# Kernel optimization log

Hardware: AMD Instinct MI355X
Metric: run time of the kernel (lower is better)

The kernel has to match this reference:

```python
import jax, jax.numpy as jnp
import numpy as np

EPS = 1e-12  # torch F.normalize eps


def setup_inputs() -> dict:
    key = jax.random.key(0)
    ks = jax.random.split(key, 6)
    B, D, C, N = 4096, 512, 17, 100000
    return {
        "feature": jax.random.normal(ks[0], (B, D), dtype=jnp.float32),
        "clf_w": jax.random.normal(ks[1], (C, D), dtype=jnp.float32),
        "clf_b": jax.random.normal(ks[2], (C,), dtype=jnp.float32),
        "supports": jax.random.normal(ks[3], (N, D), dtype=jnp.float32),
        "ent_bank": jax.random.uniform(ks[4], (N,), dtype=jnp.float32),
        "labels_idx": jax.random.randint(ks[5], (N,), 0, C, dtype=jnp.int64),
        "filter_K": 2048,
    }


def reference(feature, clf_w, clf_b, supports, ent_bank, labels_idx, filter_K):
    C = clf_w.shape[0]
    # classifier logits on the incoming batch
    p = feature @ clf_w.T + clf_b                       # [B, C]
    logp = jax.nn.log_softmax(p, axis=1)
    ent_new = -jnp.sum(jnp.exp(logp) * logp, axis=1)    # softmax entropy [B]
    yhat_idx = jnp.argmax(p, axis=1)                    # pseudo-labels [B]

    # grow the support bank
    sup = jnp.concatenate([supports, feature], axis=0)              # [N+B, D]
    y_hat = jnp.concatenate([labels_idx.astype(jnp.int32),
                             yhat_idx.astype(jnp.int32)], axis=0)   # [N+B]
    ent = jnp.concatenate([ent_bank, ent_new], axis=0)              # [N+B]

    # normalize supports once (select-then-normalize == normalize-then-select)
    sup_n = sup / jnp.maximum(jnp.linalg.norm(sup, axis=1, keepdims=True), EPS)

    # per-class lowest-entropy top-K select; one-hot labels make
    # supports.T @ labels a per-class sum of selected normalized supports.
    def per_class(c):
        ent_c = jnp.where(y_hat == c, ent, jnp.inf)
        neg_top, idx = jax.lax.top_k(-ent_c, filter_K)   # K smallest entropies
        valid = jnp.isfinite(neg_top).astype(sup_n.dtype)  # class may have < K
        return jnp.sum(sup_n[idx] * valid[:, None], axis=0)  # [D]

    Wc = jax.vmap(per_class)(jnp.arange(C))             # [C, D]
    weights = Wc.T                                      # [D, C]
    w_norm = weights / jnp.maximum(jnp.linalg.norm(weights, axis=0, keepdims=True), EPS)
    return feature @ w_norm                             # [B, C]
```

## Files before the change

### kernel.cpp

```cpp
#include <hip/hip_runtime.h>
#include <math.h>
#include <limits.h>

#define D 512
#define C 17
#define CAP 2048
#define CANDCAP 2048
#define PAD 64

__global__ __launch_bounds__(256) void k_front(
    const float* __restrict__ feature, const float* __restrict__ clf_w,
    const float* __restrict__ clf_b, const float* __restrict__ ent_bank,
    const int* __restrict__ labels, float* __restrict__ ent_new,
    int* __restrict__ yhat, unsigned* __restrict__ hist16,
    unsigned* __restrict__ ghist8, int N, int B)
{
    __shared__ float w_s[C * D];
    __shared__ float b_s[C];
    int tid = threadIdx.x;
    for (int i = tid; i < C * D; i += 256) w_s[i] = clf_w[i];
    if (tid < C) b_s[tid] = clf_b[tid];
    __syncthreads();
    int wave = tid >> 6, lane = tid & 63;

    int row = blockIdx.x * 4 + wave;
    if (row < B) {
        const float* f = feature + (size_t)row * D;
        float4 f0 = *(const float4*)(f + lane * 8);
        float4 f1 = *(const float4*)(f + lane * 8 + 4);
        double p[C];
        for (int c = 0; c < C; ++c) {
            const float* w = w_s + c * D + lane * 8;
            double s = (double)f0.x * w[0] + (double)f0.y * w[1] +
                       (double)f0.z * w[2] + (double)f0.w * w[3] +
                       (double)f1.x * w[4] + (double)f1.y * w[5] +
                       (double)f1.z * w[6] + (double)f1.w * w[7];
            for (int m = 32; m; m >>= 1) s += __shfl_xor(s, m, 64);
            p[c] = s + (double)b_s[c];
        }
        if (lane == 0) {
            double mx = p[0]; int am = 0;
            for (int c = 1; c < C; ++c) if (p[c] > mx) { mx = p[c]; am = c; }
            double Z = 0.0, S = 0.0;
            for (int c = 0; c < C; ++c) {
                double e = exp(p[c] - mx);
                Z += e; S += e * (p[c] - mx);
            }
            float ent = (float)(log(Z) - S / Z);
            ent_new[row] = ent;
            yhat[row] = am;
            unsigned b = __float_as_uint(ent);
            atomicAdd(&hist16[(size_t)am * 65536 + (b >> 16)], 1u);
            atomicAdd(&ghist8[am * 256 + (b >> 24)], 1u);
        }
    }

    int gtid = blockIdx.x * 256 + tid;
    int nchunk = N >> 2;
    if (gtid < nchunk) {
        int4 y4 = *(const int4*)(labels + gtid * 4);
        float4 e4 = *(const float4*)(ent_bank + gtid * 4);
        unsigned b;
        b = __float_as_uint(e4.x);
        atomicAdd(&hist16[(size_t)y4.x * 65536 + (b >> 16)], 1u);
        atomicAdd(&ghist8[y4.x * 256 + (b >> 24)], 1u);
        b = __float_as_uint(e4.y);
        atomicAdd(&hist16[(size_t)y4.y * 65536 + (b >> 16)], 1u);
        atomicAdd(&ghist8[y4.y * 256 + (b >> 24)], 1u);
        b = __float_as_uint(e4.z);
        atomicAdd(&hist16[(size_t)y4.z * 65536 + (b >> 16)], 1u);
        atomicAdd(&ghist8[y4.z * 256 + (b >> 24)], 1u);
        b = __float_as_uint(e4.w);
        atomicAdd(&hist16[(size_t)y4.w * 65536 + (b >> 16)], 1u);
        atomicAdd(&ghist8[y4.w * 256 + (b >> 24)], 1u);
    }
    if (blockIdx.x == 0) {
        for (int i = (nchunk << 2) + tid; i < N; i += 256) {
            int y = labels[i];
            unsigned b = __float_as_uint(ent_bank[i]);
            atomicAdd(&hist16[(size_t)y * 65536 + (b >> 16)], 1u);
            atomicAdd(&ghist8[y * 256 + (b >> 24)], 1u);
        }
    }
}

__device__ inline void wave_rank256(const unsigned h[4], int K, int lane,
                                    int* out_bin, int* out_excl, unsigned* out_total)
{
    unsigned lsum = h[0] + h[1] + h[2] + h[3];
    unsigned x = lsum;
    for (int off = 1; off < 64; off <<= 1) {
        unsigned t = __shfl_up(x, off, 64);
        if (lane >= off) x += t;
    }
    *out_total = __shfl((int)x, 63, 64);
    unsigned excl = x - lsum;
    int myb = -1; int mye = 0;
    unsigned run = excl;
    for (int k = 0; k < 4; ++k) {
        unsigned inc = run + h[k];
        if ((int)run < K && K <= (int)inc) { myb = lane * 4 + k; mye = (int)run; }
        run = inc;
    }
    unsigned long long m = __ballot(myb >= 0);
    int src = (int)__ffsll((unsigned long long)m) - 1;
    *out_bin  = __shfl(myb, src, 64);
    *out_excl = __shfl(mye, src, 64);
}

__global__ __launch_bounds__(256) void k_compact(
    const float* __restrict__ ent_bank, const int* __restrict__ labels,
    const float* __restrict__ ent_new, const int* __restrict__ yhat,
    const unsigned* __restrict__ ghist8, const unsigned* __restrict__ hist16,
    const int* __restrict__ fk, int* __restrict__ krem_g,
    int* __restrict__ cnt_g, int* __restrict__ list,
    unsigned* __restrict__ ccnt_g, unsigned* __restrict__ candb,
    int* __restrict__ candi, int N, int B)
{
    __shared__ unsigned pfx16[C];
    __shared__ int krem_s[C];
    __shared__ int done_s[C];
    __shared__ int lcnt[C], lofs[C], lput[C], gbase[C];
    __shared__ int l_list[1024 + 8];

    int tid = threadIdx.x, wave = tid >> 6, lane = tid & 63;
    int K = fk[0];

    for (int c = wave; c < C; c += 4) {
        uint4 g0 = *(const uint4*)(ghist8 + c * 256 + lane * 4);
        unsigned h[4] = { g0.x, g0.y, g0.z, g0.w };
        int chunk, e1; unsigned total;
        wave_rank256(h, K, lane, &chunk, &e1, &total);
        if ((int)total <= K) {
            if (lane == 0) { done_s[c] = 1; krem_s[c] = 0; pfx16[c] = 0xFFFFFFFFu; }
            continue;
        }
        int K2 = K - e1;
        uint4 g1 = *(const uint4*)(hist16 + (size_t)c * 65536 + chunk * 256 + lane * 4);
        unsigned h2[4] = { g1.x, g1.y, g1.z, g1.w };
        int bin, e2; unsigned tot2;
        wave_rank256(h2, K2, lane, &bin, &e2, &tot2);
        if (lane == 0) {
            done_s[c] = 0;
            pfx16[c] = (unsigned)(chunk * 256 + bin);
            krem_s[c] = K2 - e2;
        }
    }
    if (tid < C) { lcnt[tid] = 0; }
    __syncthreads();
    if (blockIdx.x == 0 && tid < C) krem_g[tid] = krem_s[tid];

    int NT = N + B;
    int nchunk = NT >> 2;
    int gtid = blockIdx.x * 256 + tid;
    int4 y4; uint4 b4; int i0 = gtid << 2; int vn = 0;
    if (gtid < nchunk) {
        vn = 4;
        if (i0 + 4 <= N) {
            y4 = *(const int4*)(labels + i0);
            float4 e = *(const float4*)(ent_bank + i0);
            b4 = make_uint4(__float_as_uint(e.x), __float_as_uint(e.y),
                            __float_as_uint(e.z), __float_as_uint(e.w));
        } else if (i0 >= N) {
            y4 = *(const int4*)(yhat + (i0 - N));
            float4 e = *(const float4*)(ent_new + (i0 - N));
            b4 = make_uint4(__float_as_uint(e.x), __float_as_uint(e.y),
                            __float_as_uint(e.z), __float_as_uint(e.w));
        } else {
            int ys[4]; unsigned bs[4];
            for (int k = 0; k < 4; ++k) {
                int i = i0 + k;
                ys[k] = (i < N) ? labels[i] : yhat[i - N];
                bs[k] = __float_as_uint((i < N) ? ent_bank[i] : ent_new[i - N]);
            }
            y4 = make_int4(ys[0], ys[1], ys[2], ys[3]);
            b4 = make_uint4(bs[0], bs[1], bs[2], bs[3]);
        }
    }
    int y_t = 0; unsigned b_t = 0; int i_t = 0; int have_t = 0;
    int tail0 = nchunk << 2;
    if (blockIdx.x == 0 && tail0 + tid < NT) {
        i_t = tail0 + tid;
        y_t = (i_t < N) ? labels[i_t] : yhat[i_t - N];
        b_t = __float_as_uint((i_t < N) ? ent_bank[i_t] : ent_new[i_t - N]);
        have_t = 1;
    }

    auto each = [&](auto&& g) {
        if (vn > 0) { g(y4.x, b4.x, i0 + 0); g(y4.y, b4.y, i0 + 1);
                      g(y4.z, b4.z, i0 + 2); g(y4.w, b4.w, i0 + 3); }
        if (have_t) g(y_t, b_t, i_t);
    };

    each([&](int y, unsigned b, int i) {
        (void)i;
        unsigned t16 = b >> 16;
        if (done_s[y] || t16 < pfx16[y]) atomicAdd(&lcnt[y], 1);
    });
    __syncthreads();
    if (tid == 0) {
        int run = 0;
        for (int c = 0; c < C; ++c) { lofs[c] = run; run += lcnt[c]; }
    }
    __syncthreads();
    if (tid < C) {
        gbase[tid] = atomicAdd(&cnt_g[tid * PAD], lcnt[tid]);
        lput[tid] = lofs[tid];
    }
    __syncthreads();
    each([&](int y, unsigned b, int i) {
        unsigned t16 = b >> 16;
        if (done_s[y] || t16 < pfx16[y]) {
            int p = atomicAdd(&lput[y], 1);
            l_list[p] = i;
        } else if (t16 == pfx16[y]) {
            unsigned q = atomicAdd(&ccnt_g[y * PAD], 1u);
            if (q < CANDCAP) { candb[y * CANDCAP + q] = b; candi[y * CANDCAP + q] = i; }
        }
    });
    __syncthreads();
    for (int c = 0; c < C; ++c) {
        int m = lcnt[c], base = gbase[c], off = lofs[c];
        for (int t = tid; t < m; t += 256)
            list[c * CAP + base + t] = l_list[off + t];
    }
}

__global__ __launch_bounds__(256) void k_accum(
    const float* __restrict__ supports, const float* __restrict__ feature,
    const int* __restrict__ list, const int* __restrict__ cnt_g,
    const unsigned* __restrict__ ccnt_g, const unsigned* __restrict__ candb,
    const int* __restrict__ candi, const int* __restrict__ krem_g,
    float* __restrict__ Wc, int N)
{
    __shared__ float wsum[4][D];
    __shared__ unsigned cb_s[CANDCAP];
    __shared__ int ci_s[CANDCAP];
    __shared__ int win[CANDCAP];
    __shared__ int wn_s;

    int c = blockIdx.y;
    int s = min(cnt_g[c * PAD], CAP);
    int nch = gridDim.x;
    int R = (s + nch - 1) / nch;
    int start = blockIdx.x * R;
    int end = min(start + R, s);
    int lane = threadIdx.x & 63, wave = threadIdx.x >> 6;
    float a0 = 0.f, a1 = 0.f, a2 = 0.f, a3 = 0.f;
    float a4 = 0.f, a5 = 0.f, a6 = 0.f, a7 = 0.f;

    auto add_row = [&](int r) {
        const float* x = (r < N) ? (supports + (size_t)r * D)
                                 : (feature + (size_t)(r - N) * D);
        float4 p = *(const float4*)(x + lane * 8);
        float4 q = *(const float4*)(x + lane * 8 + 4);
        float ss = p.x * p.x + p.y * p.y + p.z * p.z + p.w * p.w +
                   q.x * q.x + q.y * q.y + q.z * q.z + q.w * q.w;
        for (int m = 32; m; m >>= 1) ss += __shfl_xor(ss, m, 64);
        float inv = 1.f / fmaxf(sqrtf(ss), 1e-12f);
        a0 += p.x * inv; a1 += p.y * inv; a2 += p.z * inv; a3 += p.w * inv;
        a4 += q.x * inv; a5 += q.y * inv; a6 += q.z * inv; a7 += q.w * inv;
    };

    for (int j = start + wave; j < end; j += 4) add_row(list[c * CAP + j]);

    if (blockIdx.x == 0) {
        int n = (int)min(ccnt_g[c * PAD], (unsigned)CANDCAP);
        int Kr = krem_g[c];
        if (n > 0 && Kr > 0) {
            if (threadIdx.x == 0) wn_s = 0;
            for (int j = threadIdx.x; j < n; j += 256) {
                cb_s[j] = candb[c * CANDCAP + j];
                ci_s[j] = candi[c * CANDCAP + j];
            }
            __syncthreads();
            for (int j = threadIdx.x; j < n; j += 256) {
                unsigned bj = cb_s[j]; int ij = ci_s[j];
                int r = 0;
                for (int k = 0; k < n; ++k) {
                    unsigned bk = cb_s[k]; int ik = ci_s[k];
                    r += (bk < bj || (bk == bj && ik < ij)) ? 1 : 0;
                }
                if (r < Kr) { int pos = atomicAdd(&wn_s, 1); win[pos] = ij; }
            }
            __syncthreads();
            int wn = wn_s;
            for (int j = wave; j < wn; j += 4) add_row(win[j]);
        }
    }

    *(float4*)&wsum[wave][lane * 8]     = make_float4(a0, a1, a2, a3);
    *(float4*)&wsum[wave][lane * 8 + 4] = make_float4(a4, a5, a6, a7);
    __syncthreads();
    for (int i = threadIdx.x; i < D; i += 256) {
        float t = wsum[0][i] + wsum[1][i] + wsum[2][i] + wsum[3][i];
        if (t != 0.f) atomicAdd(&Wc[c * D + i], t);
    }
}

__global__ __launch_bounds__(256) void k_out(
    const float* __restrict__ feature, const float* __restrict__ Wc,
    float* __restrict__ out, int B)
{
    __shared__ float w_s[C * D];
    __shared__ float inv_s[C];
    int tid = threadIdx.x;
    for (int i = tid; i < C * D; i += 256) w_s[i] = Wc[i];
    __syncthreads();
    int wave = tid >> 6, lane = tid & 63;
    for (int c = wave; c < C; c += 4) {
        const float* w = w_s + c * D + lane * 8;
        float ss = 0.f;
        for (int k = 0; k < 8; ++k) ss += w[k] * w[k];
        for (int m = 32; m; m >>= 1) ss += __shfl_xor(ss, m, 64);
        if (lane == 0) inv_s[c] = 1.f / fmaxf(sqrtf(ss), 1e-12f);
    }
    __syncthreads();
    for (int row = blockIdx.x * 4 + wave; row < B; row += gridDim.x * 4) {
        const float* f = feature + (size_t)row * D;
        float4 f0 = *(const float4*)(f + lane * 8);
        float4 f1 = *(const float4*)(f + lane * 8 + 4);
        for (int c = 0; c < C; ++c) {
            const float* w = w_s + c * D + lane * 8;
            float s = f0.x * w[0] + f0.y * w[1] + f0.z * w[2] + f0.w * w[3] +
                      f1.x * w[4] + f1.y * w[5] + f1.z * w[6] + f1.w * w[7];
            for (int m = 32; m; m >>= 1) s += __shfl_xor(s, m, 64);
            if (lane == 0) out[(size_t)row * C + c] = s * inv_s[c];
        }
    }
}

extern "C" void kernel_launch(void* const* d_in, const int* in_sizes, int n_in,
                              void* d_out, int out_size, void* d_ws, size_t ws_size,
                              hipStream_t stream)
{
    (void)n_in; (void)out_size; (void)ws_size;
    const float* feature  = (const float*)d_in[0];
    const float* clf_w    = (const float*)d_in[1];
    const float* clf_b    = (const float*)d_in[2];
    const float* supports = (const float*)d_in[3];
    const float* ent_bank = (const float*)d_in[4];
    const int*   labels   = (const int*)d_in[5];
    const int*   fk       = (const int*)d_in[6];
    int B  = in_sizes[0] / D;
    int N  = in_sizes[4];
    int NT = N + B;

    char* ws = (char*)d_ws;
    size_t o = 0;
    auto align256 = [&](size_t x) { return (x + 255) & ~(size_t)255; };
    unsigned* hist16  = (unsigned*)(ws + o); o = align256(o + (size_t)C * 65536 * 4);
    unsigned* ghist8  = (unsigned*)(ws + o); o = align256(o + (size_t)C * 256 * 4);
    float*    Wc      = (float*)(ws + o);    o = align256(o + (size_t)C * D * 4);
    int*      cnt_g   = (int*)(ws + o);      o = align256(o + (size_t)C * PAD * 4);
    unsigned* ccnt_g  = (unsigned*)(ws + o); o = align256(o + (size_t)C * PAD * 4);
    size_t zero_bytes = o;
    float*    ent_new = (float*)(ws + o);    o = align256(o + (size_t)B * 4);
    int*      yhat    = (int*)(ws + o);      o = align256(o + (size_t)B * 4);
    int*      krem_g  = (int*)(ws + o);      o = align256(o + 32 * 4);
    int*      list    = (int*)(ws + o);      o = align256(o + (size_t)C * CAP * 4);
    unsigned* candb   = (unsigned*)(ws + o); o = align256(o + (size_t)C * CANDCAP * 4);
    int*      candi   = (int*)(ws + o);      o = align256(o + (size_t)C * CANDCAP * 4);
    float*    out     = (float*)d_out;

    hipMemsetAsync(ws, 0, zero_bytes, stream);

    int cb = (B + 3) / 4; if (cb > 1024) cb = 1024;
    int fb = cb; int bankb = ((N >> 2) + 255) / 256; if (bankb > fb) fb = bankb;
    int sgc = ((NT >> 2) + 255) / 256;

    k_front<<<fb, 256, 0, stream>>>(feature, clf_w, clf_b, ent_bank, labels,
                                    ent_new, yhat, hist16, ghist8, N, B);
    k_compact<<<sgc, 256, 0, stream>>>(ent_bank, labels, ent_new, yhat,
                                       ghist8, hist16, fk, krem_g,
                                       cnt_g, list, ccnt_g, candb, candi, N, B);
    k_accum<<<dim3(32, C), 256, 0, stream>>>(supports, feature, list, cnt_g,
                                             ccnt_g, candb, candi, krem_g, Wc, N);
    k_out<<<cb, 256, 0, stream>>>(feature, Wc, out, B);
}
```

Before: 359.4 us.

## Fuse pipeline into single cooperative kernel with grid-wide syncs

Replaces the four separate launches (front, compact, accum, out) with one cooperative kernel of 256 persistent blocks separated by grid.sync barriers. It also keeps the coarse 8-bit histogram in shared memory per block and flushes it with one atomic per nonzero bin. Boundary-candidate selection moves into its own phase, where one block per class ranks candidates in parallel into a second list. The final output stage normalizes the class weights once in shared memory, in two halves. The aim is to cut launch gaps and global atomic contention, at the cost of limiting parallelism to a fixed grid and adding grid-wide barrier overhead. The old multi-kernel path remains as a fallback if the cooperative launch fails.

```diff
diff --git a/kernel.cpp b/kernel.cpp
--- a/kernel.cpp
+++ b/kernel.cpp
@@ -1,12 +1,342 @@
 #include <hip/hip_runtime.h>
+#include <hip/hip_cooperative_groups.h>
 #include <math.h>
-#include <limits.h>
+
+namespace cg = cooperative_groups;
 
 #define D 512
 #define C 17
 #define CAP 2048
 #define CANDCAP 2048
 #define PAD 64
+#define GRID 256
+
+__device__ inline void wave_rank256(const unsigned h[4], int K, int lane,
+                                    int* out_bin, int* out_excl, unsigned* out_total)
+{
+    unsigned lsum = h[0] + h[1] + h[2] + h[3];
+    unsigned x = lsum;
+    for (int off = 1; off < 64; off <<= 1) {
+        unsigned t = __shfl_up(x, off, 64);
+        if (lane >= off) x += t;
+    }
+    *out_total = __shfl((int)x, 63, 64);
+    unsigned excl = x - lsum;
+    int myb = -1; int mye = 0;
+    unsigned run = excl;
+    for (int k = 0; k < 4; ++k) {
+        unsigned inc = run + h[k];
+        if ((int)run < K && K <= (int)inc) { myb = lane * 4 + k; mye = (int)run; }
+        run = inc;
+    }
+    unsigned long long m = __ballot(myb >= 0);
+    int src = (int)__ffsll((unsigned long long)m) - 1;
+    *out_bin  = __shfl(myb, src, 64);
+    *out_excl = __shfl(mye, src, 64);
+}
+
+struct KParams {
+    const float* feature; const float* clf_w; const float* clf_b;
+    const float* supports; const float* ent_bank; const int* labels;
+    const int* fk;
+    float* ent_new; int* yhat;
+    unsigned* hist16; unsigned* ghist8; float* Wc;
+    int* cnt_g; unsigned* ccnt_g; int* krem_g; int* s2cnt;
+    int* list; int* list2; unsigned* candb; int* candi;
+    float* out; int N; int B;
+};
+
+union SMem {
+    struct { unsigned h8[C * 256]; } p1;
+    struct { unsigned pfx16[C]; int krem_s[C]; int done_s[C];
+             int lcnt[C]; int lofs[C]; int lput[C]; int gbase[C];
+             int l_list[1312]; } p2;
+    struct { unsigned cb[CANDCAP]; int ci[CANDCAP]; } p3;
+    struct { float wsum[4][D]; } p4;
+    struct { float w_s[9 * D]; float inv_s[32]; } p5;
+};
+
+__global__ __launch_bounds__(256, 1) void k_fused(KParams P)
+{
+    cg::grid_group grid = cg::this_grid();
+    __shared__ SMem sm;
+
+    const int tid = threadIdx.x, bid = blockIdx.x;
+    const int gtid = bid * 256 + tid;
+    const int gsz = GRID * 256;
+    const int wave = tid >> 6, lane = tid & 63;
+    const int gwave = bid * 4 + wave, nwave = GRID * 4;
+    const int N = P.N, B = P.B, NT = N + B;
+
+    {
+        for (int i = tid; i < C * 256; i += 256) sm.p1.h8[i] = 0;
+        __syncthreads();
+
+        for (int row = gwave; row < B; row += nwave) {
+            const float* f = P.feature + (size_t)row * D;
+            float4 f0 = *(const float4*)(f + lane * 8);
+            float4 f1 = *(const float4*)(f + lane * 8 + 4);
+            double p[C];
+            for (int c = 0; c < C; ++c) {
+                const float* w = P.clf_w + c * D + lane * 8;
+                double s = (double)f0.x * w[0] + (double)f0.y * w[1] +
+                           (double)f0.z * w[2] + (double)f0.w * w[3] +
+                           (double)f1.x * w[4] + (double)f1.y * w[5] +
+                           (double)f1.z * w[6] + (double)f1.w * w[7];
+                for (int m = 32; m; m >>= 1) s += __shfl_xor(s, m, 64);
+                p[c] = s + (double)P.clf_b[c];
+            }
+            if (lane == 0) {
+                double mx = p[0]; int am = 0;
+                for (int c = 1; c < C; ++c) if (p[c] > mx) { mx = p[c]; am = c; }
+                double Z = 0.0, S = 0.0;
+                for (int c = 0; c < C; ++c) {
+                    double e = exp(p[c] - mx);
+                    Z += e; S += e * (p[c] - mx);
+                }
+                float ent = (float)(log(Z) - S / Z);
+                P.ent_new[row] = ent;
+                P.yhat[row] = am;
+                unsigned b = __float_as_uint(ent);
+                atomicAdd(&P.hist16[(size_t)am * 65536 + (b >> 16)], 1u);
+                atomicAdd(&P.ghist8[am * 256 + (b >> 24)], 1u);
+            }
+        }
+
+        int nbch = N >> 2;
+        for (int j = gtid; j < nbch; j += gsz) {
+            int4 y4 = *(const int4*)(P.labels + j * 4);
+            float4 e4 = *(const float4*)(P.ent_bank + j * 4);
+            unsigned b;
+            b = __float_as_uint(e4.x);
+            atomicAdd(&P.hist16[(size_t)y4.x * 65536 + (b >> 16)], 1u);
+            atomicAdd(&sm.p1.h8[y4.x * 256 + (b >> 24)], 1u);
+            b = __float_as_uint(e4.y);
+            atomicAdd(&P.hist16[(size_t)y4.y * 65536 + (b >> 16)], 1u);
+            atomicAdd(&sm.p1.h8[y4.y * 256 + (b >> 24)], 1u);
+            b = __float_as_uint(e4.z);
+            atomicAdd(&P.hist16[(size_t)y4.z * 65536 + (b >> 16)], 1u);
+            atomicAdd(&sm.p1.h8[y4.z * 256 + (b >> 24)], 1u);
+            b = __float_as_uint(e4.w);
+            atomicAdd(&P.hist16[(size_t)y4.w * 65536 + (b >> 16)], 1u);
+            atomicAdd(&sm.p1.h8[y4.w * 256 + (b >> 24)], 1u);
+        }
+        if (bid == 0) {
+            for (int i = (nbch << 2) + tid; i < N; i += 256) {
+                int y = P.labels[i];
+                unsigned b = __float_as_uint(P.ent_bank[i]);
+                atomicAdd(&P.hist16[(size_t)y * 65536 + (b >> 16)], 1u);
+                atomicAdd(&P.ghist8[y * 256 + (b >> 24)], 1u);
+            }
+        }
+        __syncthreads();
+        for (int i = tid; i < C * 256; i += 256) {
+            unsigned v = sm.p1.h8[i];
+            if (v) atomicAdd(&P.ghist8[i], v);
+        }
+    }
+    __threadfence(); grid.sync(); __threadfence();
+
+    {
+        int K = P.fk[0];
+        for (int c = wave; c < C; c += 4) {
+            uint4 g0 = *(const uint4*)(P.ghist8 + c * 256 + lane * 4);
+            unsigned h[4] = { g0.x, g0.y, g0.z, g0.w };
+            int chunk, e1; unsigned total;
+            wave_rank256(h, K, lane, &chunk, &e1, &total);
+            if ((int)total <= K) {
+                if (lane == 0) { sm.p2.done_s[c] = 1; sm.p2.krem_s[c] = 0;
+                                 sm.p2.pfx16[c] = 0xFFFFFFFFu; }
+                continue;
+            }
+            int K2 = K - e1;
+            uint4 g1 = *(const uint4*)(P.hist16 + (size_t)c * 65536 + chunk * 256 + lane * 4);
+            unsigned h2[4] = { g1.x, g1.y, g1.z, g1.w };
+            int bin, e2; unsigned tot2;
+            wave_rank256(h2, K2, lane, &bin, &e2, &tot2);
+            if (lane == 0) {
+                sm.p2.done_s[c] = 0;
+                sm.p2.pfx16[c] = (unsigned)(chunk * 256 + bin);
+                sm.p2.krem_s[c] = K2 - e2;
+            }
+        }
+        if (tid < C) sm.p2.lcnt[tid] = 0;
+        __syncthreads();
+        if (bid == 0 && tid < C) P.krem_g[tid] = sm.p2.krem_s[tid];
+
+        int nchunk = NT >> 2;
+        int4 y4; uint4 b4; int i0 = gtid << 2; int vn = 0;
+        if (gtid < nchunk) {
+            vn = 4;
+            if (i0 + 4 <= N) {
+                y4 = *(const int4*)(P.labels + i0);
+                float4 e = *(const float4*)(P.ent_bank + i0);
+                b4 = make_uint4(__float_as_uint(e.x), __float_as_uint(e.y),
+                                __float_as_uint(e.z), __float_as_uint(e.w));
+            } else if (i0 >= N) {
+                y4 = *(const int4*)(P.yhat + (i0 - N));
+                float4 e = *(const float4*)(P.ent_new + (i0 - N));
+                b4 = make_uint4(__float_as_uint(e.x), __float_as_uint(e.y),
+                                __float_as_uint(e.z), __float_as_uint(e.w));
+            } else {
+                int ys[4]; unsigned bs[4];
+                for (int k = 0; k < 4; ++k) {
+                    int i = i0 + k;
+                    ys[k] = (i < N) ? P.labels[i] : P.yhat[i - N];
+                    bs[k] = __float_as_uint((i < N) ? P.ent_bank[i] : P.ent_new[i - N]);
+                }
+                y4 = make_int4(ys[0], ys[1], ys[2], ys[3]);
+                b4 = make_uint4(bs[0], bs[1], bs[2], bs[3]);
+            }
+        }
+        int y_t = 0; unsigned b_t = 0; int i_t = 0; int have_t = 0;
+        int tail0 = nchunk << 2;
+        if (bid == 0 && tail0 + tid < NT) {
+            i_t = tail0 + tid;
+            y_t = (i_t < N) ? P.labels[i_t] : P.yhat[i_t - N];
+            b_t = __float_as_uint((i_t < N) ? P.ent_bank[i_t] : P.ent_new[i_t - N]);
+            have_t = 1;
+        }
+        auto each = [&](auto&& g) {
+            if (vn > 0) { g(y4.x, b4.x, i0 + 0); g(y4.y, b4.y, i0 + 1);
+                          g(y4.z, b4.z, i0 + 2); g(y4.w, b4.w, i0 + 3); }
+            if (have_t) g(y_t, b_t, i_t);
+        };
+
+        each([&](int y, unsigned b, int i) {
+            (void)i;
+            unsigned t16 = b >> 16;
+            if (sm.p2.done_s[y] || t16 < sm.p2.pfx16[y]) atomicAdd(&sm.p2.lcnt[y], 1);
+        });
+        __syncthreads();
+        if (tid == 0) {
+            int run = 0;
+            for (int c = 0; c < C; ++c) { sm.p2.lofs[c] = run; run += sm.p2.lcnt[c]; }
+        }
+        __syncthreads();
+        if (tid < C) {
+            int m = sm.p2.lcnt[tid];
+            sm.p2.gbase[tid] = m ? atomicAdd(&P.cnt_g[tid * PAD], m) : 0;
+            sm.p2.lput[tid] = sm.p2.lofs[tid];
+        }
+        __syncthreads();
+        each([&](int y, unsigned b, int i) {
+            unsigned t16 = b >> 16;
+            if (sm.p2.done_s[y] || t16 < sm.p2.pfx16[y]) {
+                int p = atomicAdd(&sm.p2.lput[y], 1);
+                sm.p2.l_list[p] = i;
+            } else if (t16 == sm.p2.pfx16[y]) {
+                unsigned q = atomicAdd(&P.ccnt_g[y * PAD], 1u);
+                if (q < CANDCAP) { P.candb[y * CANDCAP + q] = b;
+                                   P.candi[y * CANDCAP + q] = i; }
+            }
+        });
+        __syncthreads();
+        for (int c = 0; c < C; ++c) {
+            int m = sm.p2.lcnt[c], base = sm.p2.gbase[c], off = sm.p2.lofs[c];
+            int lim = CAP - base; if (m > lim) m = lim;
+            for (int t = tid; t < m; t += 256)
+                P.list[c * CAP + base + t] = sm.p2.l_list[off + t];
+        }
+    }
+    __threadfence(); grid.sync(); __threadfence();
+
+    if (bid < C) {
+        int c = bid;
+        int Kr = P.krem_g[c];
+        int n = (int)min(P.ccnt_g[c * PAD], (unsigned)CANDCAP);
+        if (Kr > 0 && n > 0) {
+            for (int j = tid; j < n; j += 256) {
+                sm.p3.cb[j] = __hip_atomic_load(&P.candb[c * CANDCAP + j],
+                                  __ATOMIC_RELAXED, __HIP_MEMORY_SCOPE_AGENT);
+                sm.p3.ci[j] = __hip_atomic_load(&P.candi[c * CANDCAP + j],
+                                  __ATOMIC_RELAXED, __HIP_MEMORY_SCOPE_AGENT);
+            }
+            __syncthreads();
+            for (int j = tid; j < n; j += 256) {
+                unsigned bj = sm.p3.cb[j]; int ij = sm.p3.ci[j];
+                int r = 0;
+                for (int k = 0; k < n; ++k) {
+                    unsigned bk = sm.p3.cb[k]; int ik = sm.p3.ci[k];
+                    r += (bk < bj || (bk == bj && ik < ij)) ? 1 : 0;
+                }
+                if (r < Kr) P.list2[c * CANDCAP + r] = ij;
+            }
+        }
+        if (tid == 0) P.s2cnt[c] = (Kr > 0) ? min(Kr, n) : 0;
+    }
+    __threadfence(); grid.sync(); __threadfence();
+
+    {
+        int c = bid % C;
+        int q = bid / C;
+        int nch = (GRID - c + C - 1) / C;
+        int s = min(P.cnt_g[c * PAD], CAP);
+        int R = (s + nch - 1) / nch;
+        int start = q * R;
+        int end = min(start + R, s);
+        float a0 = 0.f, a1 = 0.f, a2 = 0.f, a3 = 0.f;
+        float a4 = 0.f, a5 = 0.f, a6 = 0.f, a7 = 0.f;
+        auto add_row = [&](int r) {
+            const float* x = (r < N) ? (P.supports + (size_t)r * D)
+                                     : (P.feature + (size_t)(r - N) * D);
+            float4 pp = *(const float4*)(x + lane * 8);
+            float4 qq = *(const float4*)(x + lane * 8 + 4);
+            float ss = pp.x * pp.x + pp.y * pp.y + pp.z * pp.z + pp.w * pp.w +
+                       qq.x * qq.x + qq.y * qq.y + qq.z * qq.z + qq.w * qq.w;
+            for (int m = 32; m; m >>= 1) ss += __shfl_xor(ss, m, 64);
+            float inv = 1.f / fmaxf(sqrtf(ss), 1e-12f);
+            a0 += pp.x * inv; a1 += pp.y * inv; a2 += pp.z * inv; a3 += pp.w * inv;
+            a4 += qq.x * inv; a5 += qq.y * inv; a6 += qq.z * inv; a7 += qq.w * inv;
+        };
+        const int* lp = P.list + c * CAP;
+        for (int j = start + wave; j < end; j += 4) add_row(lp[j]);
+        if (q == 0) {
+            int s2 = P.s2cnt[c];
+            for (int j = wave; j < s2; j += 4) add_row(P.list2[c * CANDCAP + j]);
+        }
+        *(float4*)&sm.p4.wsum[wave][lane * 8]     = make_float4(a0, a1, a2, a3);
+        *(float4*)&sm.p4.wsum[wave][lane * 8 + 4] = make_float4(a4, a5, a6, a7);
+        __syncthreads();
+        for (int i = tid; i < D; i += 256) {
+            float t = sm.p4.wsum[0][i] + sm.p4.wsum[1][i] +
+                      sm.p4.wsum[2][i] + sm.p4.wsum[3][i];
+            if (t != 0.f) atomicAdd(&P.Wc[c * D + i], t);
+        }
+    }
+    __threadfence(); grid.sync(); __threadfence();
+
+    {
+        for (int c = wave; c < C; c += 4) {
+            const float* w = P.Wc + c * D + lane * 8;
+            float ss = 0.f;
+            for (int k = 0; k < 8; ++k) ss += w[k] * w[k];
+            for (int m = 32; m; m >>= 1) ss += __shfl_xor(ss, m, 64);
+            if (lane == 0) sm.p5.inv_s[c] = 1.f / fmaxf(sqrtf(ss), 1e-12f);
+        }
+        __syncthreads();
+        for (int half = 0; half < 2; ++half) {
+            int c0 = half * 9, c1 = (half == 0) ? 9 : C;
+            int nc = c1 - c0;
+            for (int i = tid; i < nc * D; i += 256)
+                sm.p5.w_s[i] = P.Wc[c0 * D + i] * sm.p5.inv_s[c0 + i / D];
+            __syncthreads();
+            for (int row = gwave; row < B; row += nwave) {
+                const float* f = P.feature + (size_t)row * D;
+                float4 f0 = *(const float4*)(f + lane * 8);
+                float4 f1 = *(const float4*)(f + lane * 8 + 4);
+                for (int c = 0; c < nc; ++c) {
+                    const float* w = sm.p5.w_s + c * D + lane * 8;
+                    float s = f0.x * w[0] + f0.y * w[1] + f0.z * w[2] + f0.w * w[3] +
+                              f1.x * w[4] + f1.y * w[5] + f1.z * w[6] + f1.w * w[7];
+                    for (int m = 32; m; m >>= 1) s += __shfl_xor(s, m, 64);
+                    if (lane == 0) P.out[(size_t)row * C + c0 + c] = s;
+                }
+            }
+            __syncthreads();
+        }
+    }
+}
 
 __global__ __launch_bounds__(256) void k_front(
     const float* __restrict__ feature, const float* __restrict__ clf_w,
@@ -16,13 +346,12 @@
     unsigned* __restrict__ ghist8, int N, int B)
 {
     __shared__ float w_s[C * D];
-    __shared__ float b_s[C];
+    __shared__ float b_s[32];
     int tid = threadIdx.x;
     for (int i = tid; i < C * D; i += 256) w_s[i] = clf_w[i];
     if (tid < C) b_s[tid] = clf_b[tid];
     __syncthreads();
     int wave = tid >> 6, lane = tid & 63;
-
     int row = blockIdx.x * 4 + wave;
     if (row < B) {
         const float* f = feature + (size_t)row * D;
@@ -54,7 +383,6 @@
             atomicAdd(&ghist8[am * 256 + (b >> 24)], 1u);
         }
     }
-
     int gtid = blockIdx.x * 256 + tid;
     int nchunk = N >> 2;
     if (gtid < nchunk) {
@@ -84,30 +412,6 @@
     }
 }
 
-__device__ inline void wave_rank256(const unsigned h[4], int K, int lane,
-                                    int* out_bin, int* out_excl, unsigned* out_total)
-{
-    unsigned lsum = h[0] + h[1] + h[2] + h[3];
-    unsigned x = lsum;
-    for (int off = 1; off < 64; off <<= 1) {
-        unsigned t = __shfl_up(x, off, 64);
-        if (lane >= off) x += t;
-    }
-    *out_total = __shfl((int)x, 63, 64);
-    unsigned excl = x - lsum;
-    int myb = -1; int mye = 0;
-    unsigned run = excl;
-    for (int k = 0; k < 4; ++k) {
-        unsigned inc = run + h[k];
-        if ((int)run < K && K <= (int)inc) { myb = lane * 4 + k; mye = (int)run; }
-        run = inc;
-    }
-    unsigned long long m = __ballot(myb >= 0);
-    int src = (int)__ffsll((unsigned long long)m) - 1;
-    *out_bin  = __shfl(myb, src, 64);
-    *out_excl = __shfl(mye, src, 64);
-}
-
 __global__ __launch_bounds__(256) void k_compact(
     const float* __restrict__ ent_bank, const int* __restrict__ labels,
     const float* __restrict__ ent_new, const int* __restrict__ yhat,
@@ -121,11 +425,10 @@
     __shared__ int krem_s[C];
     __shared__ int done_s[C];
     __shared__ int lcnt[C], lofs[C], lput[C], gbase[C];
-    __shared__ int l_list[1024 + 8];
+    __shared__ int l_list[1312];
 
     int tid = threadIdx.x, wave = tid >> 6, lane = tid & 63;
     int K = fk[0];
-
     for (int c = wave; c < C; c += 4) {
         uint4 g0 = *(const uint4*)(ghist8 + c * 256 + lane * 4);
         unsigned h[4] = { g0.x, g0.y, g0.z, g0.w };
@@ -146,7 +449,7 @@
             krem_s[c] = K2 - e2;
         }
     }
-    if (tid < C) { lcnt[tid] = 0; }
+    if (tid < C) lcnt[tid] = 0;
     __syncthreads();
     if (blockIdx.x == 0 && tid < C) krem_g[tid] = krem_s[tid];
 
@@ -185,13 +488,11 @@
         b_t = __float_as_uint((i_t < N) ? ent_bank[i_t] : ent_new[i_t - N]);
         have_t = 1;
     }
-
     auto each = [&](auto&& g) {
         if (vn > 0) { g(y4.x, b4.x, i0 + 0); g(y4.y, b4.y, i0 + 1);
                       g(y4.z, b4.z, i0 + 2); g(y4.w, b4.w, i0 + 3); }
         if (have_t) g(y_t, b_t, i_t);
     };
-
     each([&](int y, unsigned b, int i) {
         (void)i;
         unsigned t16 = b >> 16;
@@ -204,7 +505,8 @@
     }
     __syncthreads();
     if (tid < C) {
-        gbase[tid] = atomicAdd(&cnt_g[tid * PAD], lcnt[tid]);
+        int m = lcnt[tid];
+        gbase[tid] = m ? atomicAdd(&cnt_g[tid * PAD], m) : 0;
         lput[tid] = lofs[tid];
     }
     __syncthreads();
@@ -221,6 +523,7 @@
     __syncthreads();
     for (int c = 0; c < C; ++c) {
         int m = lcnt[c], base = gbase[c], off = lofs[c];
+        int lim = CAP - base; if (m > lim) m = lim;
         for (int t = tid; t < m; t += 256)
             list[c * CAP + base + t] = l_list[off + t];
     }
@@ -248,7 +551,6 @@
     int lane = threadIdx.x & 63, wave = threadIdx.x >> 6;
     float a0 = 0.f, a1 = 0.f, a2 = 0.f, a3 = 0.f;
     float a4 = 0.f, a5 = 0.f, a6 = 0.f, a7 = 0.f;
-
     auto add_row = [&](int r) {
         const float* x = (r < N) ? (supports + (size_t)r * D)
                                  : (feature + (size_t)(r - N) * D);
@@ -261,9 +563,7 @@
         a0 += p.x * inv; a1 += p.y * inv; a2 += p.z * inv; a3 += p.w * inv;
         a4 += q.x * inv; a5 += q.y * inv; a6 += q.z * inv; a7 += q.w * inv;
     };
-
     for (int j = start + wave; j < end; j += 4) add_row(list[c * CAP + j]);
-
     if (blockIdx.x == 0) {
         int n = (int)min(ccnt_g[c * PAD], (unsigned)CANDCAP);
         int Kr = krem_g[c];
@@ -288,7 +588,6 @@
             for (int j = wave; j < wn; j += 4) add_row(win[j]);
         }
     }
-
     *(float4*)&wsum[wave][lane * 8]     = make_float4(a0, a1, a2, a3);
     *(float4*)&wsum[wave][lane * 8 + 4] = make_float4(a4, a5, a6, a7);
     __syncthreads();
@@ -303,7 +602,7 @@
     float* __restrict__ out, int B)
 {
     __shared__ float w_s[C * D];
-    __shared__ float inv_s[C];
+    __shared__ float inv_s[32];
     int tid = threadIdx.x;
     for (int i = tid; i < C * D; i += 256) w_s[i] = Wc[i];
     __syncthreads();
@@ -358,23 +657,33 @@
     float*    ent_new = (float*)(ws + o);    o = align256(o + (size_t)B * 4);
     int*      yhat    = (int*)(ws + o);      o = align256(o + (size_t)B * 4);
     int*      krem_g  = (int*)(ws + o);      o = align256(o + 32 * 4);
+    int*      s2cnt   = (int*)(ws + o);      o = align256(o + 32 * 4);
     int*      list    = (int*)(ws + o);      o = align256(o + (size_t)C * CAP * 4);
+    int*      list2   = (int*)(ws + o);      o = align256(o + (size_t)C * CANDCAP * 4);
     unsigned* candb   = (unsigned*)(ws + o); o = align256(o + (size_t)C * CANDCAP * 4);
     int*      candi   = (int*)(ws + o);      o = align256(o + (size_t)C * CANDCAP * 4);
     float*    out     = (float*)d_out;
 
     hipMemsetAsync(ws, 0, zero_bytes, stream);
 
-    int cb = (B + 3) / 4; if (cb > 1024) cb = 1024;
-    int fb = cb; int bankb = ((N >> 2) + 255) / 256; if (bankb > fb) fb = bankb;
-    int sgc = ((NT >> 2) + 255) / 256;
-
-    k_front<<<fb, 256, 0, stream>>>(feature, clf_w, clf_b, ent_bank, labels,
-                                    ent_new, yhat, hist16, ghist8, N, B);
-    k_compact<<<sgc, 256, 0, stream>>>(ent_bank, labels, ent_new, yhat,
-                                       ghist8, hist16, fk, krem_g,
-                                       cnt_g, list, ccnt_g, candb, candi, N, B);
-    k_accum<<<dim3(32, C), 256, 0, stream>>>(supports, feature, list, cnt_g,
-                                             ccnt_g, candb, candi, krem_g, Wc, N);
-    k_out<<<cb, 256, 0, stream>>>(feature, Wc, out, B);
+    KParams P = { feature, clf_w, clf_b, supports, ent_bank, labels, fk,
+                  ent_new, yhat, hist16, ghist8, Wc,
+                  cnt_g, ccnt_g, krem_g, s2cnt,
+                  list, list2, candb, candi, out, N, B };
+    void* args[] = { (void*)&P };
+    hipError_t e = hipLaunchCooperativeKernel((const void*)k_fused, dim3(GRID),
+                                              dim3(256), args, 0, stream);
+    if (e != hipSuccess) {
+        int cb = (B + 3) / 4; if (cb > 1024) cb = 1024;
+        int fb = cb; int bankb = ((N >> 2) + 255) / 256; if (bankb > fb) fb = bankb;
+        int sgc = ((NT >> 2) + 255) / 256;
+        k_front<<<fb, 256, 0, stream>>>(feature, clf_w, clf_b, ent_bank, labels,
+                                        ent_new, yhat, hist16, ghist8, N, B);
+        k_compact<<<sgc, 256, 0, stream>>>(ent_bank, labels, ent_new, yhat,
+                                           ghist8, hist16, fk, krem_g,
+                                           cnt_g, list, ccnt_g, candb, candi, N, B);
+        k_accum<<<dim3(32, C), 256, 0, stream>>>(supports, feature, list, cnt_g,
+                                                 ccnt_g, candb, candi, krem_g, Wc, N);
+        k_out<<<cb, 256, 0, stream>>>(feature, Wc, out, B);
+    }
 }
```

Result: slower. 644.3 us (+79.3%).
